# Optimization experiments

Hardware: AMD Instinct MI355X
Metric: run time of the kernel (lower is better)

Reference implementation:

```python
import jax, jax.numpy as jnp
import numpy as np

B, S, E = 2, 2048, 1024
H = 16
HD = E // H           # 64
KD = 64               # k_dim
VD = 64               # v_dim
SCALE = 1.0 / np.float32(np.sqrt(KD))


def setup_inputs() -> dict:
    key = jax.random.key(0)
    ks = jax.random.split(key, 10)
    return {
        "x": jax.random.normal(ks[0], (B, S, E), dtype=jnp.float32),
        "mask": jax.random.uniform(ks[1], (S, S), dtype=jnp.float32),
        "Wq": jax.random.normal(ks[2], (HD, KD), dtype=jnp.float32) * 0.05,
        "bq": jax.random.normal(ks[3], (KD,), dtype=jnp.float32) * 0.05,
        "Wk": jax.random.normal(ks[4], (HD, KD), dtype=jnp.float32) * 0.05,
        "bk": jax.random.normal(ks[5], (KD,), dtype=jnp.float32) * 0.05,
        "Wv": jax.random.normal(ks[6], (HD, VD), dtype=jnp.float32) * 0.05,
        "bv": jax.random.normal(ks[7], (VD,), dtype=jnp.float32) * 0.05,
        "Wo": jax.random.normal(ks[8], (H * VD, E), dtype=jnp.float32) * 0.05,
        "bo": jax.random.normal(ks[9], (E,), dtype=jnp.float32) * 0.05,
    }


def reference(x, mask, Wq, bq, Wk, bk, Wv, bv, Wo, bo):
    b, s, e = x.shape
    # (B, S, E) -> (B, H, S, head_dim)
    xh = x.reshape(b, s, H, HD).transpose(0, 2, 1, 3)
    q = jnp.einsum('bhsd,dk->bhsk', xh, Wq) + bq   # (B,H,S,KD)
    k = jnp.einsum('bhsd,dk->bhsk', xh, Wk) + bk   # (B,H,S,KD)
    v = jnp.einsum('bhsd,dv->bhsv', xh, Wv) + bv   # (B,H,S,VD)
    sim = jnp.einsum('bhqk,bhsk->bhqs', q, k) * SCALE  # (B,H,S,S)
    sim = sim * mask[None, None, :, :]                  # multiplicative mask
    attn = jax.nn.softmax(sim, axis=-1)
    out = jnp.einsum('bhqs,bhsv->bhqv', attn, v)        # (B,H,S,VD)
    out = out.transpose(0, 2, 1, 3).reshape(b, s, H * VD)
    return out @ Wo + bo
```

## Files before the change

### kernel.cpp

```cpp
#include <hip/hip_runtime.h>
#include <hip/hip_bf16.h>

#define SS 2048
#define EE 1024
#define SCALE 0.125f
#define LOG2E 1.44269504088896f

typedef __attribute__((ext_vector_type(8))) short short8;
typedef __attribute__((ext_vector_type(4))) float float4v;
typedef __attribute__((ext_vector_type(8))) unsigned short ushort8;
typedef __attribute__((ext_vector_type(4))) unsigned int uint4v;

__device__ __forceinline__ float bf2f(unsigned short u) {
  unsigned int v = ((unsigned int)u) << 16;
  return __uint_as_float(v);
}
__device__ __forceinline__ unsigned short f2bf(float f) {
  unsigned int u = __float_as_uint(f);
  unsigned int lsb = (u >> 16) & 1u;
  u += 0x7fffu + lsb;
  return (unsigned short)(u >> 16);
}
__device__ __forceinline__ unsigned int pk2bf(float a, float b) {
  __hip_bfloat162 h = __float22bfloat162_rn(float2{a, b});
  return *reinterpret_cast<unsigned int*>(&h);
}

__global__ __launch_bounds__(256) void w3t_prep(
    const float* __restrict__ Wq, const float* __restrict__ Wk,
    const float* __restrict__ Wv, unsigned short* __restrict__ W3T)
{
  __shared__ unsigned short t[64 * 65];
  const float* W = (blockIdx.x == 0) ? Wq : (blockIdx.x == 1 ? Wk : Wv);
  int tid = threadIdx.x;
#pragma unroll
  for (int i = 0; i < 16; ++i) {
    int e = tid + i * 256; int d = e >> 6, n = e & 63;
    t[n * 65 + d] = f2bf(W[e]);
  }
  __syncthreads();
  unsigned short* dst = W3T + blockIdx.x * 4096;
#pragma unroll
  for (int i = 0; i < 16; ++i) {
    int e = tid + i * 256; int n = e >> 6, d = e & 63;
    dst[n * 64 + d] = t[n * 65 + d];
  }
}

__global__ __launch_bounds__(256) void qkv_kernel(
    const float* __restrict__ x, const unsigned short* __restrict__ W3T,
    const float* __restrict__ bq, const float* __restrict__ bk,
    const float* __restrict__ bv,
    unsigned short* __restrict__ Q, unsigned short* __restrict__ K,
    unsigned short* __restrict__ Vp)
{
  __shared__ __align__(16) unsigned short w3t[192 * 72];
  __shared__ __align__(16) unsigned short xt[64 * 72];
  __shared__ float sBias[192];
  int tid = threadIdx.x;
  int bh = blockIdx.x >> 4;
  int s0blk = (blockIdx.x & 15) * 128;
  int b = bh >> 4, h = bh & 15;
  int wv = tid >> 6, lane = tid & 63;
  int li = lane & 15, g = lane >> 4;

#pragma unroll
  for (int i = 0; i < 6; ++i) {
    int slot = tid + i * 256;
    int row = slot >> 3, c = slot & 7;
    *(short8*)(w3t + row * 72 + c * 8) = *(const short8*)(W3T + slot * 8);
  }
  if (tid < 192) sBias[tid] = (tid < 64) ? bq[tid] : (tid < 128 ? bk[tid - 64] : bv[tid - 128]);

  for (int half = 0; half < 2; ++half) {
    int s0 = s0blk + half * 64;
    if (half) __syncthreads();
    const float* xbase = x + ((size_t)(b * SS + s0)) * EE + h * 64;
#pragma unroll
    for (int it = 0; it < 4; ++it) {
      int flat = tid + it * 256;
      int row = flat >> 4, ch = flat & 15;
      float4 v = *(const float4*)(xbase + (size_t)row * EE + ch * 4);
      uint2 u; u.x = pk2bf(v.x, v.y); u.y = pk2bf(v.z, v.w);
      *(uint2*)(xt + row * 72 + ch * 4) = u;
    }
    __syncthreads();

    int mrow = wv * 16;
    short8 af[2];
#pragma unroll
    for (int ks = 0; ks < 2; ++ks)
      af[ks] = *(const short8*)(xt + (mrow + li) * 72 + ks * 32 + g * 8);

    float4v acc[12];
#pragma unroll
    for (int i = 0; i < 12; ++i) acc[i] = (float4v){0, 0, 0, 0};
#pragma unroll
    for (int ks = 0; ks < 2; ++ks)
#pragma unroll
      for (int nb = 0; nb < 12; ++nb) {
        short8 bfr = *(const short8*)(w3t + (nb * 16 + li) * 72 + ks * 32 + g * 8);
        acc[nb] = __builtin_amdgcn_mfma_f32_16x16x32_bf16(af[ks], bfr, acc[nb], 0, 0, 0);
      }

    int srow0 = s0 + mrow + g * 4;
#pragma unroll
    for (int nb = 0; nb < 12; ++nb) {
      float bias = sBias[nb * 16 + li];
      int mtx = nb >> 2, sub = nb & 3;
#pragma unroll
      for (int r = 0; r < 4; ++r) {
        unsigned short ob = f2bf(acc[nb][r] + bias);
        int s = srow0 + r;
        if (mtx == 0)      Q[((size_t)bh * SS + s) * 64 + sub * 16 + li] = ob;
        else if (mtx == 1) K[((size_t)bh * SS + s) * 64 + sub * 16 + li] = ob;
        else {
          int sl = s & 31;
          int pos = ((sl >> 2) & 3) * 8 + ((sl >> 4) & 1) * 4 + (sl & 3);
          Vp[(size_t)bh * 131072 + (size_t)(s >> 5) * 2048 + (sub * 16 + li) * 32 + pos] = ob;
        }
      }
    }
  }
}

__global__ __launch_bounds__(256) void mask_prep(
    const float* __restrict__ mask, unsigned short* __restrict__ maskP)
{
  int idx = blockIdx.x * 256 + threadIdx.x;
  int lane = idx & 63, step = (idx >> 6) & 63, qt = idx >> 12;
  int li = lane & 15, g = lane >> 4;
  const float c = SCALE * LOG2E;
  const float* mrow = mask + (size_t)(qt * 16 + li) * SS + step * 32 + g * 4;
  float4 a = *(const float4*)mrow;
  float4 bb = *(const float4*)(mrow + 16);
  uint4v o;
  o.x = pk2bf(a.x * c, a.y * c);
  o.y = pk2bf(a.z * c, a.w * c);
  o.z = pk2bf(bb.x * c, bb.y * c);
  o.w = pk2bf(bb.z * c, bb.w * c);
  *(uint4v*)(maskP + (size_t)idx * 8) = o;
}

__global__ __launch_bounds__(256) void attn_kernel(
    const unsigned short* __restrict__ Q, const unsigned short* __restrict__ K,
    const unsigned short* __restrict__ Vp, const unsigned short* __restrict__ maskP,
    unsigned short* __restrict__ AO)
{
  __shared__ __align__(16) unsigned short lds[2 * 2816 + 2 * 2560];
  unsigned short* ktb0 = lds;
  unsigned short* ktb1 = lds + 2816;
  unsigned short* vtb0 = lds + 5632;
  unsigned short* vtb1 = lds + 8192;

  int tid = threadIdx.x, wv = tid >> 6, lane = tid & 63;
  int li = lane & 15, g = lane >> 4;
  int bh = blockIdx.x >> 5;
  int q0 = (blockIdx.x & 31) * 64 + wv * 16;

  const unsigned short* Qb = Q + ((size_t)bh * SS + q0 + li) * 64;
  short8 qf0 = *(const short8*)(Qb + g * 8);
  short8 qf1 = *(const short8*)(Qb + 32 + g * 8);

  const unsigned short* Kg = K + (size_t)bh * SS * 64 + tid * 8;
  const unsigned short* Vg = Vp + (size_t)bh * 131072 + tid * 8;
  const unsigned short* Mg = maskP + (size_t)(q0 >> 4) * 32768 + lane * 8;
  int kldso = (tid >> 3) * 88 + (tid & 7) * 8;
  int vldso = (tid >> 2) * 40 + (tid & 3) * 8;

  float4v acc[4];
#pragma unroll
  for (int nb = 0; nb < 4; ++nb) acc[nb] = (float4v){0, 0, 0, 0};
  float2 den2 = {0.f, 0.f};

  short8 kreg = *(const short8*)Kg;
  short8 vreg = *(const short8*)Vg;
  uint4v mc = *(const uint4v*)Mg;
  *(short8*)(ktb0 + kldso) = kreg;
  *(short8*)(vtb0 + vldso) = vreg;
  __syncthreads();

  for (int step = 0; step < 64; ++step) {
    const unsigned short* kt = (step & 1) ? ktb1 : ktb0;
    const unsigned short* vt = (step & 1) ? vtb1 : vtb0;
    unsigned short* ktn = (step & 1) ? ktb0 : ktb1;
    unsigned short* vtn = (step & 1) ? vtb0 : vtb1;
    int ns = (step + 1) & 63;
    kreg = *(const short8*)(Kg + (size_t)ns * 2048);
    vreg = *(const short8*)(Vg + (size_t)ns * 2048);
    uint4v mn = *(const uint4v*)(Mg + (size_t)ns * 512);

    short8 kf[2][2];
#pragma unroll
    for (int sb = 0; sb < 2; ++sb) {
      kf[sb][0] = *(const short8*)(kt + (sb * 16 + li) * 88 + g * 8);
      kf[sb][1] = *(const short8*)(kt + (sb * 16 + li) * 88 + 32 + g * 8);
    }

    uint4v pw;
#pragma unroll
    for (int sb = 0; sb < 2; ++sb) {
      float4v st = {0, 0, 0, 0};
      st = __builtin_amdgcn_mfma_f32_16x16x32_bf16(kf[sb][0], qf0, st, 0, 0, 0);
      st = __builtin_amdgcn_mfma_f32_16x16x32_bf16(kf[sb][1], qf1, st, 0, 0, 0);
#pragma unroll
      for (int hh = 0; hh < 2; ++hh) {
        unsigned int mm = mc[sb * 2 + hh];
        float mlo = __uint_as_float(mm << 16);
        float mhi = __uint_as_float(mm & 0xffff0000u);
        float p0 = __builtin_amdgcn_exp2f(st[2 * hh] * mlo);
        float p1 = __builtin_amdgcn_exp2f(st[2 * hh + 1] * mhi);
        den2.x += p0;
        den2.y += p1;
        pw[sb * 2 + hh] = pk2bf(p0, p1);
      }
    }
    short8 pf = *(short8*)&pw;
#pragma unroll
    for (int nb = 0; nb < 4; ++nb) {
      short8 vf = *(const short8*)(vt + (nb * 16 + li) * 40 + g * 8);
      acc[nb] = __builtin_amdgcn_mfma_f32_16x16x32_bf16(vf, pf, acc[nb], 0, 0, 0);
    }
    *(short8*)(ktn + kldso) = kreg;
    *(short8*)(vtn + vldso) = vreg;
    mc = mn;
    __syncthreads();
  }

  float d = den2.x + den2.y;
  d += __shfl_xor(d, 16, 64);
  d += __shfl_xor(d, 32, 64);
  float rd = 1.0f / d;

  unsigned short* tr = lds + wv * 1152;
#pragma unroll
  for (int nb = 0; nb < 4; ++nb) {
    int base = li * 72 + nb * 16 + g * 4;
    *(unsigned int*)(tr + base)     = pk2bf(acc[nb][0] * rd, acc[nb][1] * rd);
    *(unsigned int*)(tr + base + 2) = pk2bf(acc[nb][2] * rd, acc[nb][3] * rd);
  }
  asm volatile("s_waitcnt lgkmcnt(0)" ::: "memory");

  int b = bh >> 4, h = bh & 15;
  int rrow = lane >> 3, part = lane & 7;
#pragma unroll
  for (int i = 0; i < 2; ++i) {
    int row = i * 8 + rrow;
    short8 ov = *(const short8*)(tr + row * 72 + part * 8);
    *(short8*)(AO + ((size_t)(b * SS + q0 + row)) * EE + h * 64 + part * 8) = ov;
  }
}

__global__ __launch_bounds__(256) void transpose_wo(
    const float* __restrict__ Wo, unsigned short* __restrict__ WoT)
{
  __shared__ unsigned short t[64 * 65];
  int tid = threadIdx.x;
  int k0 = (blockIdx.x >> 4) * 64;
  int n0 = (blockIdx.x & 15) * 64;
#pragma unroll
  for (int i = 0; i < 16; ++i) {
    int idx = tid + i * 256;
    int k = idx >> 6, n = idx & 63;
    t[n * 65 + k] = f2bf(Wo[(size_t)(k0 + k) * 1024 + n0 + n]);
  }
  __syncthreads();
#pragma unroll
  for (int i = 0; i < 16; ++i) {
    int idx = tid + i * 256;
    int n = idx >> 6, k = idx & 63;
    WoT[(size_t)(n0 + n) * 1024 + k0 + k] = t[n * 65 + k];
  }
}

__global__ __launch_bounds__(256) void out_gemm(
    const unsigned short* __restrict__ AO, const unsigned short* __restrict__ WoT,
    const float* __restrict__ bo, float* __restrict__ out)
{
  __shared__ __align__(16) unsigned short at[128 * 72];
  __shared__ __align__(16) unsigned short bt[64 * 72];
  int tid = threadIdx.x, wv = tid >> 6, lane = tid & 63;
  int li = lane & 15, g = lane >> 4;
  int m0 = (blockIdx.x >> 4) * 128;
  int n0 = (blockIdx.x & 15) * 64;
  int wm = (wv & 1) * 64, wn = (wv >> 1) * 32;

  const unsigned short* Ag = AO + (size_t)m0 * 1024;
  const unsigned short* Bg = WoT + (size_t)n0 * 1024;
  int srow = tid >> 3, scol = (tid & 7) * 8;

  short8 apre[4], bpre[2];
  auto ldst = [&](int k0) {
#pragma unroll
    for (int i = 0; i < 4; ++i)
      apre[i] = *(const short8*)(Ag + (size_t)(srow + i * 32) * 1024 + k0 + scol);
#pragma unroll
    for (int i = 0; i < 2; ++i)
      bpre[i] = *(const short8*)(Bg + (size_t)(srow + i * 32) * 1024 + k0 + scol);
  };

  float4v acc[4][2];
#pragma unroll
  for (int mt = 0; mt < 4; ++mt)
#pragma unroll
    for (int nt = 0; nt < 2; ++nt) acc[mt][nt] = (float4v){0, 0, 0, 0};

  ldst(0);
  for (int k0 = 0; k0 < 1024; k0 += 64) {
    __syncthreads();
#pragma unroll
    for (int i = 0; i < 4; ++i)
      *(short8*)(at + (srow + i * 32) * 72 + scol) = apre[i];
#pragma unroll
    for (int i = 0; i < 2; ++i)
      *(short8*)(bt + (srow + i * 32) * 72 + scol) = bpre[i];
    int nk = (k0 + 64 < 1024) ? k0 + 64 : 0;
    ldst(nk);
    __syncthreads();
#pragma unroll
    for (int ks = 0; ks < 2; ++ks) {
      short8 afr[4], bfr[2];
#pragma unroll
      for (int mt = 0; mt < 4; ++mt)
        afr[mt] = *(const short8*)(at + (wm + mt * 16 + li) * 72 + ks * 32 + g * 8);
#pragma unroll
      for (int nt = 0; nt < 2; ++nt)
        bfr[nt] = *(const short8*)(bt + (wn + nt * 16 + li) * 72 + ks * 32 + g * 8);
#pragma unroll
      for (int mt = 0; mt < 4; ++mt)
#pragma unroll
        for (int nt = 0; nt < 2; ++nt)
          acc[mt][nt] = __builtin_amdgcn_mfma_f32_16x16x32_bf16(afr[mt], bfr[nt], acc[mt][nt], 0, 0, 0);
    }
  }
#pragma unroll
  for (int nt = 0; nt < 2; ++nt) {
    float bof = bo[n0 + wn + nt * 16 + li];
#pragma unroll
    for (int mt = 0; mt < 4; ++mt)
#pragma unroll
      for (int r = 0; r < 4; ++r)
        out[(size_t)(m0 + wm + mt * 16 + g * 4 + r) * 1024 + n0 + wn + nt * 16 + li] =
            acc[mt][nt][r] + bof;
  }
}

extern "C" void kernel_launch(void* const* d_in, const int* in_sizes, int n_in,
                              void* d_out, int out_size, void* d_ws, size_t ws_size,
                              hipStream_t stream) {
  const float* x    = (const float*)d_in[0];
  const float* mask = (const float*)d_in[1];
  const float* Wq   = (const float*)d_in[2];
  const float* bq   = (const float*)d_in[3];
  const float* Wk   = (const float*)d_in[4];
  const float* bk   = (const float*)d_in[5];
  const float* Wv   = (const float*)d_in[6];
  const float* bv   = (const float*)d_in[7];
  const float* Wo   = (const float*)d_in[8];
  const float* bo   = (const float*)d_in[9];
  float* out = (float*)d_out;

  unsigned short* ws = (unsigned short*)d_ws;
  unsigned short* Q     = ws;
  unsigned short* K     = ws + 4194304;
  unsigned short* Vp    = ws + 8388608;
  unsigned short* AO    = ws + 12582912;
  unsigned short* maskP = ws + 16777216;
  unsigned short* W3T = AO;
  unsigned short* WoT = maskP;

  w3t_prep<<<3, 256, 0, stream>>>(Wq, Wk, Wv, W3T);
  qkv_kernel<<<512, 256, 0, stream>>>(x, W3T, bq, bk, bv, Q, K, Vp);
  mask_prep<<<2048, 256, 0, stream>>>(mask, maskP);
  attn_kernel<<<1024, 256, 0, stream>>>(Q, K, Vp, maskP, AO);
  transpose_wo<<<256, 256, 0, stream>>>(Wo, WoT);
  out_gemm<<<512, 256, 0, stream>>>(AO, WoT, bo, out);
}
```

Before: 192.7 us.

## Pre-swizzle K/V into fragment order, MFMA denominator, merge prep kernels

The QKV kernel now writes K and V directly in MFMA fragment order, so the attention kernel stages them into LDS with flat contiguous copies and reads each fragment as one contiguous 16-byte load per lane, without padded strided addressing. The softmax denominator is computed by an extra MFMA against a ones vector in place of per-lane adds and cross-lane shuffles. The mask-prep and weight-prep kernels are merged into one launch. This trades scattered global writes in qkv_kernel and one extra MFMA per step for simpler LDS access and one fewer launch; the unpadded LDS layout may introduce bank conflicts.

```diff
diff --git a/kernel.cpp b/kernel.cpp
--- a/kernel.cpp
+++ b/kernel.cpp
@@ -8,13 +8,8 @@
 
 typedef __attribute__((ext_vector_type(8))) short short8;
 typedef __attribute__((ext_vector_type(4))) float float4v;
-typedef __attribute__((ext_vector_type(8))) unsigned short ushort8;
 typedef __attribute__((ext_vector_type(4))) unsigned int uint4v;
 
-__device__ __forceinline__ float bf2f(unsigned short u) {
-  unsigned int v = ((unsigned int)u) << 16;
-  return __uint_as_float(v);
-}
 __device__ __forceinline__ unsigned short f2bf(float f) {
   unsigned int u = __float_as_uint(f);
   unsigned int lsb = (u >> 16) & 1u;
@@ -26,20 +21,40 @@
   return *reinterpret_cast<unsigned int*>(&h);
 }
 
-__global__ __launch_bounds__(256) void w3t_prep(
+__global__ __launch_bounds__(256) void prep_kernel(
+    const float* __restrict__ mask,
     const float* __restrict__ Wq, const float* __restrict__ Wk,
-    const float* __restrict__ Wv, unsigned short* __restrict__ W3T)
+    const float* __restrict__ Wv,
+    unsigned short* __restrict__ maskP, unsigned short* __restrict__ W3T)
 {
   __shared__ unsigned short t[64 * 65];
-  const float* W = (blockIdx.x == 0) ? Wq : (blockIdx.x == 1 ? Wk : Wv);
+  int blk = blockIdx.x;
   int tid = threadIdx.x;
+  if (blk < 2048) {
+    int idx = blk * 256 + tid;
+    int lane = idx & 63, step = (idx >> 6) & 63, qt = idx >> 12;
+    int li = lane & 15, g = lane >> 4;
+    const float c = SCALE * LOG2E;
+    const float* mrow = mask + (size_t)(qt * 16 + li) * SS + step * 32 + g * 4;
+    float4 a = *(const float4*)mrow;
+    float4 bb = *(const float4*)(mrow + 16);
+    uint4v o;
+    o.x = pk2bf(a.x * c, a.y * c);
+    o.y = pk2bf(a.z * c, a.w * c);
+    o.z = pk2bf(bb.x * c, bb.y * c);
+    o.w = pk2bf(bb.z * c, bb.w * c);
+    *(uint4v*)(maskP + (size_t)idx * 8) = o;
+    return;
+  }
+  int m = blk - 2048;
+  const float* W = (m == 0) ? Wq : (m == 1 ? Wk : Wv);
 #pragma unroll
   for (int i = 0; i < 16; ++i) {
     int e = tid + i * 256; int d = e >> 6, n = e & 63;
     t[n * 65 + d] = f2bf(W[e]);
   }
   __syncthreads();
-  unsigned short* dst = W3T + blockIdx.x * 4096;
+  unsigned short* dst = W3T + m * 4096;
 #pragma unroll
   for (int i = 0; i < 16; ++i) {
     int e = tid + i * 256; int n = e >> 6, d = e & 63;
@@ -51,8 +66,8 @@
     const float* __restrict__ x, const unsigned short* __restrict__ W3T,
     const float* __restrict__ bq, const float* __restrict__ bk,
     const float* __restrict__ bv,
-    unsigned short* __restrict__ Q, unsigned short* __restrict__ K,
-    unsigned short* __restrict__ Vp)
+    unsigned short* __restrict__ Q, unsigned short* __restrict__ Kp,
+    unsigned short* __restrict__ Vf)
 {
   __shared__ __align__(16) unsigned short w3t[192 * 72];
   __shared__ __align__(16) unsigned short xt[64 * 72];
@@ -112,47 +127,32 @@
       for (int r = 0; r < 4; ++r) {
         unsigned short ob = f2bf(acc[nb][r] + bias);
         int s = srow0 + r;
-        if (mtx == 0)      Q[((size_t)bh * SS + s) * 64 + sub * 16 + li] = ob;
-        else if (mtx == 1) K[((size_t)bh * SS + s) * 64 + sub * 16 + li] = ob;
-        else {
+        int step = s >> 5;
+        if (mtx == 0) {
+          Q[((size_t)bh * SS + s) * 64 + sub * 16 + li] = ob;
+        } else if (mtx == 1) {
+          int sb = (s >> 4) & 1, lik = s & 15;
+          int part = sub >> 1;
+          int gk = ((sub & 1) << 1) | (li >> 3);
+          Kp[(size_t)bh * 131072 + step * 2048 + (sb * 2 + part) * 512 +
+             (gk * 16 + lik) * 8 + (li & 7)] = ob;
+        } else {
           int sl = s & 31;
           int pos = ((sl >> 2) & 3) * 8 + ((sl >> 4) & 1) * 4 + (sl & 3);
-          Vp[(size_t)bh * 131072 + (size_t)(s >> 5) * 2048 + (sub * 16 + li) * 32 + pos] = ob;
+          Vf[(size_t)bh * 131072 + step * 2048 + sub * 512 +
+             ((pos >> 3) * 16 + li) * 8 + (pos & 7)] = ob;
         }
       }
     }
   }
 }
 
-__global__ __launch_bounds__(256) void mask_prep(
-    const float* __restrict__ mask, unsigned short* __restrict__ maskP)
-{
-  int idx = blockIdx.x * 256 + threadIdx.x;
-  int lane = idx & 63, step = (idx >> 6) & 63, qt = idx >> 12;
-  int li = lane & 15, g = lane >> 4;
-  const float c = SCALE * LOG2E;
-  const float* mrow = mask + (size_t)(qt * 16 + li) * SS + step * 32 + g * 4;
-  float4 a = *(const float4*)mrow;
-  float4 bb = *(const float4*)(mrow + 16);
-  uint4v o;
-  o.x = pk2bf(a.x * c, a.y * c);
-  o.y = pk2bf(a.z * c, a.w * c);
-  o.z = pk2bf(bb.x * c, bb.y * c);
-  o.w = pk2bf(bb.z * c, bb.w * c);
-  *(uint4v*)(maskP + (size_t)idx * 8) = o;
-}
-
 __global__ __launch_bounds__(256) void attn_kernel(
-    const unsigned short* __restrict__ Q, const unsigned short* __restrict__ K,
-    const unsigned short* __restrict__ Vp, const unsigned short* __restrict__ maskP,
+    const unsigned short* __restrict__ Q, const unsigned short* __restrict__ Kp,
+    const unsigned short* __restrict__ Vf, const unsigned short* __restrict__ maskP,
     unsigned short* __restrict__ AO)
 {
-  __shared__ __align__(16) unsigned short lds[2 * 2816 + 2 * 2560];
-  unsigned short* ktb0 = lds;
-  unsigned short* ktb1 = lds + 2816;
-  unsigned short* vtb0 = lds + 5632;
-  unsigned short* vtb1 = lds + 8192;
-
+  __shared__ __align__(16) unsigned short lds[8192];
   int tid = threadIdx.x, wv = tid >> 6, lane = tid & 63;
   int li = lane & 15, g = lane >> 4;
   int bh = blockIdx.x >> 5;
@@ -162,75 +162,82 @@
   short8 qf0 = *(const short8*)(Qb + g * 8);
   short8 qf1 = *(const short8*)(Qb + 32 + g * 8);
 
-  const unsigned short* Kg = K + (size_t)bh * SS * 64 + tid * 8;
-  const unsigned short* Vg = Vp + (size_t)bh * 131072 + tid * 8;
+  const unsigned short* Kg = Kp + (size_t)bh * 131072 + tid * 8;
+  const unsigned short* Vg = Vf + (size_t)bh * 131072 + tid * 8;
   const unsigned short* Mg = maskP + (size_t)(q0 >> 4) * 32768 + lane * 8;
-  int kldso = (tid >> 3) * 88 + (tid & 7) * 8;
-  int vldso = (tid >> 2) * 40 + (tid & 3) * 8;
+
+  unsigned short ov = (li == 0) ? (unsigned short)0x3F80 : (unsigned short)0;
+  short8 vones = {(short)ov, (short)ov, (short)ov, (short)ov,
+                  (short)ov, (short)ov, (short)ov, (short)ov};
 
   float4v acc[4];
 #pragma unroll
   for (int nb = 0; nb < 4; ++nb) acc[nb] = (float4v){0, 0, 0, 0};
-  float2 den2 = {0.f, 0.f};
+  float4v accd = {0, 0, 0, 0};
 
   short8 kreg = *(const short8*)Kg;
   short8 vreg = *(const short8*)Vg;
   uint4v mc = *(const uint4v*)Mg;
-  *(short8*)(ktb0 + kldso) = kreg;
-  *(short8*)(vtb0 + vldso) = vreg;
+  *(short8*)(lds + tid * 8) = kreg;
+  *(short8*)(lds + 2048 + tid * 8) = vreg;
   __syncthreads();
 
   for (int step = 0; step < 64; ++step) {
-    const unsigned short* kt = (step & 1) ? ktb1 : ktb0;
-    const unsigned short* vt = (step & 1) ? vtb1 : vtb0;
-    unsigned short* ktn = (step & 1) ? ktb0 : ktb1;
-    unsigned short* vtn = (step & 1) ? vtb0 : vtb1;
+    const unsigned short* ktc = lds + ((step & 1) ? 4096 : 0);
+    const unsigned short* vtc = ktc + 2048;
+    unsigned short* ktn = lds + ((step & 1) ? 0 : 4096);
+    unsigned short* vtn = ktn + 2048;
     int ns = (step + 1) & 63;
     kreg = *(const short8*)(Kg + (size_t)ns * 2048);
     vreg = *(const short8*)(Vg + (size_t)ns * 2048);
     uint4v mn = *(const uint4v*)(Mg + (size_t)ns * 512);
 
-    short8 kf[2][2];
-#pragma unroll
-    for (int sb = 0; sb < 2; ++sb) {
-      kf[sb][0] = *(const short8*)(kt + (sb * 16 + li) * 88 + g * 8);
-      kf[sb][1] = *(const short8*)(kt + (sb * 16 + li) * 88 + 32 + g * 8);
-    }
+    short8 kf00 = *(const short8*)(ktc + lane * 8);
+    short8 kf01 = *(const short8*)(ktc + 512 + lane * 8);
+    short8 kf10 = *(const short8*)(ktc + 1024 + lane * 8);
+    short8 kf11 = *(const short8*)(ktc + 1536 + lane * 8);
 
     uint4v pw;
-#pragma unroll
-    for (int sb = 0; sb < 2; ++sb) {
+    {
       float4v st = {0, 0, 0, 0};
-      st = __builtin_amdgcn_mfma_f32_16x16x32_bf16(kf[sb][0], qf0, st, 0, 0, 0);
-      st = __builtin_amdgcn_mfma_f32_16x16x32_bf16(kf[sb][1], qf1, st, 0, 0, 0);
+      st = __builtin_amdgcn_mfma_f32_16x16x32_bf16(kf00, qf0, st, 0, 0, 0);
+      st = __builtin_amdgcn_mfma_f32_16x16x32_bf16(kf01, qf1, st, 0, 0, 0);
 #pragma unroll
       for (int hh = 0; hh < 2; ++hh) {
-        unsigned int mm = mc[sb * 2 + hh];
-        float mlo = __uint_as_float(mm << 16);
-        float mhi = __uint_as_float(mm & 0xffff0000u);
-        float p0 = __builtin_amdgcn_exp2f(st[2 * hh] * mlo);
-        float p1 = __builtin_amdgcn_exp2f(st[2 * hh + 1] * mhi);
-        den2.x += p0;
-        den2.y += p1;
-        pw[sb * 2 + hh] = pk2bf(p0, p1);
+        unsigned int mm = mc[hh];
+        float p0 = __builtin_amdgcn_exp2f(st[2 * hh] * __uint_as_float(mm << 16));
+        float p1 = __builtin_amdgcn_exp2f(st[2 * hh + 1] * __uint_as_float(mm & 0xffff0000u));
+        pw[hh] = pk2bf(p0, p1);
       }
     }
+    {
+      float4v st = {0, 0, 0, 0};
+      st = __builtin_amdgcn_mfma_f32_16x16x32_bf16(kf10, qf0, st, 0, 0, 0);
+      st = __builtin_amdgcn_mfma_f32_16x16x32_bf16(kf11, qf1, st, 0, 0, 0);
+#pragma unroll
+      for (int hh = 0; hh < 2; ++hh) {
+        unsigned int mm = mc[2 + hh];
+        float p0 = __builtin_amdgcn_exp2f(st[2 * hh] * __uint_as_float(mm << 16));
+        float p1 = __builtin_amdgcn_exp2f(st[2 * hh + 1] * __uint_as_float(mm & 0xffff0000u));
+        pw[2 + hh] = pk2bf(p0, p1);
+      }
+    }
     short8 pf = *(short8*)&pw;
 #pragma unroll
     for (int nb = 0; nb < 4; ++nb) {
-      short8 vf = *(const short8*)(vt + (nb * 16 + li) * 40 + g * 8);
-      acc[nb] = __builtin_amdgcn_mfma_f32_16x16x32_bf16(vf, pf, acc[nb], 0, 0, 0);
-    }
-    *(short8*)(ktn + kldso) = kreg;
-    *(short8*)(vtn + vldso) = vreg;
+      short8 vfr = *(const short8*)(vtc + nb * 512 + lane * 8);
+      acc[nb] = __builtin_amdgcn_mfma_f32_16x16x32_bf16(vfr, pf, acc[nb], 0, 0, 0);
+    }
+    accd = __builtin_amdgcn_mfma_f32_16x16x32_bf16(vones, pf, accd, 0, 0, 0);
+
+    *(short8*)(ktn + tid * 8) = kreg;
+    *(short8*)(vtn + tid * 8) = vreg;
     mc = mn;
     __syncthreads();
   }
 
-  float d = den2.x + den2.y;
-  d += __shfl_xor(d, 16, 64);
-  d += __shfl_xor(d, 32, 64);
-  float rd = 1.0f / d;
+  float den = __shfl(accd[0], li, 64);
+  float rd = 1.0f / den;
 
   unsigned short* tr = lds + wv * 1152;
 #pragma unroll
@@ -246,8 +253,8 @@
 #pragma unroll
   for (int i = 0; i < 2; ++i) {
     int row = i * 8 + rrow;
-    short8 ov = *(const short8*)(tr + row * 72 + part * 8);
-    *(short8*)(AO + ((size_t)(b * SS + q0 + row)) * EE + h * 64 + part * 8) = ov;
+    short8 o = *(const short8*)(tr + row * 72 + part * 8);
+    *(short8*)(AO + ((size_t)(b * SS + q0 + row)) * EE + h * 64 + part * 8) = o;
   }
 }
 
@@ -362,17 +369,16 @@
 
   unsigned short* ws = (unsigned short*)d_ws;
   unsigned short* Q     = ws;
-  unsigned short* K     = ws + 4194304;
-  unsigned short* Vp    = ws + 8388608;
+  unsigned short* Kp    = ws + 4194304;
+  unsigned short* Vf    = ws + 8388608;
   unsigned short* AO    = ws + 12582912;
   unsigned short* maskP = ws + 16777216;
   unsigned short* W3T = AO;
   unsigned short* WoT = maskP;
 
-  w3t_prep<<<3, 256, 0, stream>>>(Wq, Wk, Wv, W3T);
-  qkv_kernel<<<512, 256, 0, stream>>>(x, W3T, bq, bk, bv, Q, K, Vp);
-  mask_prep<<<2048, 256, 0, stream>>>(mask, maskP);
-  attn_kernel<<<1024, 256, 0, stream>>>(Q, K, Vp, maskP, AO);
+  prep_kernel<<<2051, 256, 0, stream>>>(mask, Wq, Wk, Wv, maskP, W3T);
+  qkv_kernel<<<512, 256, 0, stream>>>(x, W3T, bq, bk, bv, Q, Kp, Vf);
+  attn_kernel<<<1024, 256, 0, stream>>>(Q, Kp, Vf, maskP, AO);
   transpose_wo<<<256, 256, 0, stream>>>(Wo, WoT);
   out_gemm<<<512, 256, 0, stream>>>(AO, WoT, bo, out);
 }
```

New measurement: 189.9 us. No clear change (-1.4%).
